# Kernel optimization log

Measured on AMD Instinct MI355X. Metric: run time of the kernel, lower is better.

## Reference

```python
import jax, jax.numpy as jnp
import numpy as np

B, S, E, H = 2, 2048, 2048, 16
D = E // H  # head_dim = 128


def setup_inputs() -> dict:
    key = jax.random.key(0)
    k1, k2, k3, k4, k5 = jax.random.split(key, 5)
    hidden_states = jax.random.normal(k1, (B, S, E), dtype=jnp.float32)
    # causal mask, broadcastable to attn_shape (B, q, H, k)
    causal = jnp.tril(jnp.ones((S, S), dtype=bool))  # [q, k]
    attention_mask = jnp.broadcast_to(causal[None, :, None, :], (B, S, 1, S))
    c_attn_w = jax.random.normal(k2, (E, E + 2 * D), dtype=jnp.float32) * (E ** -0.5)
    c_attn_b = jax.random.normal(k3, (E + 2 * D,), dtype=jnp.float32) * 0.02
    c_proj_w = jax.random.normal(k4, (E, E), dtype=jnp.float32) * (E ** -0.5)
    c_proj_b = jax.random.normal(k5, (E,), dtype=jnp.float32) * 0.02
    return {
        "hidden_states": hidden_states,
        "attention_mask": attention_mask,
        "c_attn_w": c_attn_w,
        "c_attn_b": c_attn_b,
        "c_proj_w": c_proj_w,
        "c_proj_b": c_proj_b,
    }


def reference(hidden_states, attention_mask, c_attn_w, c_attn_b, c_proj_w, c_proj_b):
    b, s, e = hidden_states.shape
    h, d = H, D
    qkv = hidden_states @ c_attn_w + c_attn_b            # [b, s, e + 2d]
    query = qkv[..., :e]                                 # [b, s, e]
    key = qkv[..., e:e + d]                              # [b, s, d] (single shared KV head)
    value = qkv[..., e + d:]                             # [b, s, d]
    scale = 1.0 / (d ** 0.5)                             # scale_attn_weights, unscale=1
    q = query.reshape(b, s * h, d)
    # QK^T with MQA broadcast: [b, s*h, k]
    scores = jnp.einsum('bqd,bkd->bqk', q, key) * scale
    scores = scores.reshape(b, s, h, s)                  # attn_shape (b, q, h, k)
    mask_value = jnp.finfo(scores.dtype).min
    scores = jnp.where(attention_mask, scores, mask_value)
    probs = jax.nn.softmax(scores, axis=-1)              # fp32 softmax (upcast is no-op in fp32)
    attn = jnp.einsum('bqk,bkd->bqd', probs.reshape(b, s * h, s), value)
    attn = attn.reshape(b, s, e)
    return attn @ c_proj_w + c_proj_b
```

## Files before the change

### kernel.cpp

```cpp
#include <hip/hip_runtime.h>
#include <math.h>


typedef __attribute__((ext_vector_type(8))) short short8;
typedef __attribute__((ext_vector_type(8))) __bf16 bf16x8;
typedef __attribute__((ext_vector_type(4))) float floatx4;
typedef __attribute__((ext_vector_type(4))) unsigned short ushort4v;
typedef unsigned short ushort;

__device__ __forceinline__ ushort f2bf(float f) {
    unsigned u = __builtin_bit_cast(unsigned, f);
    u += 0x7fffu + ((u >> 16) & 1u);
    return (ushort)(u >> 16);
}
__device__ __forceinline__ unsigned pk2(float a, float b) {
    return (unsigned)f2bf(a) | ((unsigned)f2bf(b) << 16);
}

template <typename V>
__device__ __forceinline__ auto mfma_try(V a, V b, floatx4 c, int)
    -> decltype(__builtin_amdgcn_mfma_f32_16x16x32_bf16(a, b, c, 0, 0, 0)) {
    return __builtin_amdgcn_mfma_f32_16x16x32_bf16(a, b, c, 0, 0, 0);
}
template <typename V>
__device__ __forceinline__ floatx4 mfma_try(V a, V b, floatx4 c, long) {
    return __builtin_amdgcn_mfma_f32_16x16x32_bf16(
        __builtin_bit_cast(bf16x8, a), __builtin_bit_cast(bf16x8, b), c, 0, 0, 0);
}
__device__ __forceinline__ floatx4 mfma_bf16(short8 a, short8 b, floatx4 c) {
    return mfma_try(a, b, c, 0);
}

__device__ __forceinline__ void gld_lds16(const ushort* g, ushort* l) {
    __builtin_amdgcn_global_load_lds(
        (const __attribute__((address_space(1))) unsigned*)(const void*)g,
        (__attribute__((address_space(3))) unsigned*)(void*)l, 16, 0, 0);
}

__global__ __launch_bounds__(256) void convert_bf16(const float* __restrict__ X,
                                                    ushort* __restrict__ Y, int n4) {
    int i = blockIdx.x * 256 + threadIdx.x;
    if (i >= n4) return;
    float4 v = ((const float4*)X)[i];
    ushort4v o = {f2bf(v.x), f2bf(v.y), f2bf(v.z), f2bf(v.w)};
    *(ushort4v*)&Y[(size_t)i * 4] = o;
}

__global__ __launch_bounds__(256) void transpose_convert(const float* __restrict__ W,
                                                         ushort* __restrict__ WT,
                                                         int K, int N) {
    __shared__ ushort T[64][68];
    const int tid = threadIdx.x;
    const int n0 = blockIdx.x * 64, k0 = blockIdx.y * 64;
    #pragma unroll
    for (int i = 0; i < 4; ++i) {
        int k = (tid >> 4) + i * 16, n = (tid & 15) * 4;
        float4 v = *(const float4*)&W[(size_t)(k0 + k) * N + n0 + n];
        T[n + 0][k] = f2bf(v.x); T[n + 1][k] = f2bf(v.y);
        T[n + 2][k] = f2bf(v.z); T[n + 3][k] = f2bf(v.w);
    }
    __syncthreads();
    #pragma unroll
    for (int i = 0; i < 4; ++i) {
        int idx = tid + i * 256;
        int n = idx >> 4, c4 = idx & 15;
        *(ushort4v*)&WT[(size_t)(n0 + n) * K + k0 + c4 * 4] =
            *(const ushort4v*)&T[n][c4 * 4];
    }
}

__global__ __launch_bounds__(256) void v_transpose(const ushort* __restrict__ qkv,
                                                   ushort* __restrict__ VTg) {
    __shared__ ushort T[64 * 72];
    const int tid = threadIdx.x;
    const int s0 = blockIdx.x * 64, d0 = blockIdx.y * 64, b = blockIdx.z;
    const size_t bS = (size_t)b * 2048;
    #pragma unroll
    for (int i = 0; i < 2; ++i) {
        int idx = tid + i * 256;
        int s = idx >> 3, d8 = idx & 7;
        short8 v = *(const short8*)&qkv[(bS + s0 + s) * 2304 + 2176 + d0 + d8 * 8];
        #pragma unroll
        for (int j = 0; j < 8; ++j)
            T[(d8 * 8 + j) * 72 + s] = (ushort)v[j];
    }
    __syncthreads();
    #pragma unroll
    for (int i = 0; i < 2; ++i) {
        int idx = tid + i * 256;
        int d = idx >> 3, s8 = idx & 7;
        *(short8*)&VTg[((size_t)b * 128 + d0 + d) * 2048 + s0 + s8 * 8] =
            *(const short8*)&T[d * 72 + s8 * 8];
    }
}

template <int MODE>
__global__ __launch_bounds__(256) void gemm_m97(
    const ushort* __restrict__ A, const ushort* __restrict__ BT,
    const float* __restrict__ bias, void* __restrict__ C, int M, int N, int K)
{
    __shared__ ushort As[8192];
    __shared__ ushort Bs[8192];
    const int tid = threadIdx.x, lane = tid & 63, wid = tid >> 6;
    const int wr = wid >> 1, wc = wid & 1;
    const int lg = lane >> 4, li = lane & 15;
    const int m0 = blockIdx.y * 128, n0 = blockIdx.x * 128;
    const int srow = lane >> 3;
    const int sphys = (lane & 7) * 16;
    floatx4 acc[4][4] = {};

    for (int k0 = 0; k0 < K; k0 += 64) {
        __syncthreads();
        #pragma unroll
        for (int i = 0; i < 4; ++i) {
            const int c = wid * 4 + i;
            const int row = c * 8 + srow;
            const int lin = sphys ^ ((row & 7) << 4);
            gld_lds16(&A[(size_t)(m0 + row) * K + k0 + (lin >> 1)], &As[c * 512]);
            gld_lds16(&BT[(size_t)(n0 + row) * K + k0 + (lin >> 1)], &Bs[c * 512]);
        }
        __syncthreads();
        #pragma unroll
        for (int kk = 0; kk < 2; ++kk) {
            short8 af[4], bfv[4];
            const int pb = (kk * 64 + lg * 16) ^ ((li & 7) << 4);
            #pragma unroll
            for (int m = 0; m < 4; ++m)
                af[m] = *(const short8*)&As[(wr * 64 + m * 16 + li) * 64 + (pb >> 1)];
            #pragma unroll
            for (int n = 0; n < 4; ++n)
                bfv[n] = *(const short8*)&Bs[(wc * 64 + n * 16 + li) * 64 + (pb >> 1)];
            #pragma unroll
            for (int m = 0; m < 4; ++m)
                #pragma unroll
                for (int n = 0; n < 4; ++n)
                    acc[m][n] = mfma_bf16(af[m], bfv[n], acc[m][n]);
        }
    }

    #pragma unroll
    for (int m = 0; m < 4; ++m) {
        #pragma unroll
        for (int n = 0; n < 4; ++n) {
            const int col = n0 + wc * 64 + n * 16 + li;
            const float bv = bias[col];
            #pragma unroll
            for (int r = 0; r < 4; ++r) {
                const int row = m0 + wr * 64 + m * 16 + lg * 4 + r;
                float v = acc[m][n][r] + bv;
                if constexpr (MODE == 0) {
                    if (col < 2048) v *= 0.08838834764831845f;
                    ((ushort*)C)[(size_t)row * N + col] = f2bf(v);
                } else {
                    ((float*)C)[(size_t)row * N + col] = v;
                }
            }
        }
    }
}

__global__ __launch_bounds__(256, 2) void attn_kernel(
    const ushort* __restrict__ qkv,
    const ushort* __restrict__ VTg,
    ushort* __restrict__ out)
{
    constexpr int S = 2048, Dh = 128, QKV = 2304, E = 2048;
    __shared__ ushort lds[24576];
    ushort* Ks = lds;
    ushort* VT = lds + 8192;
    ushort* Ps = lds + 16384;

    const int tid = threadIdx.x, lane = tid & 63, wid = tid >> 6;
    const int lg = lane >> 4, li = lane & 15;
    const int x = blockIdx.x;
    const int st = (x & 1) ? (x >> 1) : (15 - (x >> 1));
    const int h = blockIdx.y, b = blockIdx.z;
    const size_t bS = (size_t)b * S;
    const int qA = st * 128 + wid * 16;
    const int qB = qA + 64;

    short8 qfA[4], qfB[4];
    #pragma unroll
    for (int dc = 0; dc < 4; ++dc) {
        qfA[dc] = *(const short8*)&qkv[(bS + qA + li) * QKV + h * Dh + dc * 32 + lg * 8];
        qfB[dc] = *(const short8*)&qkv[(bS + qB + li) * QKV + h * Dh + dc * 32 + lg * 8];
    }

    floatx4 oA[8] = {}, oB[8] = {};
    float mA = -1e30f, lA = 0.f, mB = -1e30f, lB = 0.f;
    const int ntiles = 2 * st + 2;

    for (int t = 0; t < ntiles; ++t) {
        const int k0 = t * 64;
        __syncthreads();
        #pragma unroll
        for (int i = 0; i < 4; ++i) {
            const int idx = tid + i * 256;
            const int row = idx >> 4, g = idx & 15;
            const int src = (g * 16) ^ ((row & 7) << 4);
            gld_lds16(&qkv[(bS + k0 + row) * QKV + E + (src >> 1)],
                      &Ks[(i * 256 + wid * 64) * 8]);
        }
        #pragma unroll
        for (int i = 0; i < 4; ++i) {
            const int idx = tid + i * 256;
            const int d = idx >> 3, kg = idx & 7;
            gld_lds16(&VTg[((size_t)b * 128 + d) * 2048 + k0 + ((kg ^ (d & 7)) << 3)],
                      &VT[(i * 256 + wid * 64) * 8]);
        }
        __syncthreads();

        floatx4 sA[4] = {{0,0,0,0},{0,0,0,0},{0,0,0,0},{0,0,0,0}};
        floatx4 sB[4] = {{0,0,0,0},{0,0,0,0},{0,0,0,0},{0,0,0,0}};
        #pragma unroll
        for (int dc = 0; dc < 4; ++dc) {
            #pragma unroll
            for (int kb = 0; kb < 4; ++kb) {
                short8 kf = *(const short8*)&Ks[(kb * 16 + li) * 128 +
                                                (((dc * 4 + lg) ^ (li & 7)) << 3)];
                sA[kb] = mfma_bf16(kf, qfA[dc], sA[kb]);
                sB[kb] = mfma_bf16(kf, qfB[dc], sB[kb]);
            }
        }
        if (t == 2 * st) {
            #pragma unroll
            for (int kb = 0; kb < 4; ++kb)
                #pragma unroll
                for (int r = 0; r < 4; ++r)
                    if (kb * 16 + lg * 4 + r > wid * 16 + li) sA[kb][r] = -1e30f;
        }
        if (t == 2 * st + 1) {
            #pragma unroll
            for (int kb = 0; kb < 4; ++kb)
                #pragma unroll
                for (int r = 0; r < 4; ++r) {
                    sA[kb][r] = -1e30f;
                    if (kb * 16 + lg * 4 + r > wid * 16 + li) sB[kb][r] = -1e30f;
                }
        }

        {
            float mt = fmaxf(fmaxf(fmaxf(sA[0][0], sA[0][1]), fmaxf(sA[0][2], sA[0][3])),
                             fmaxf(fmaxf(sA[1][0], sA[1][1]), fmaxf(sA[1][2], sA[1][3])));
            mt = fmaxf(mt, fmaxf(fmaxf(fmaxf(sA[2][0], sA[2][1]), fmaxf(sA[2][2], sA[2][3])),
                                 fmaxf(fmaxf(sA[3][0], sA[3][1]), fmaxf(sA[3][2], sA[3][3]))));
            mt = fmaxf(mt, __shfl_xor(mt, 16));
            mt = fmaxf(mt, __shfl_xor(mt, 32));
            const float mn = fmaxf(mA, mt);
            const float sc = __expf(mA - mn);
            mA = mn;
            float rs = 0.f;
            #pragma unroll
            for (int kb = 0; kb < 4; ++kb)
                #pragma unroll
                for (int r = 0; r < 4; ++r) {
                    float p = __expf(sA[kb][r] - mn);
                    sA[kb][r] = p; rs += p;
                }
            rs += __shfl_xor(rs, 16);
            rs += __shfl_xor(rs, 32);
            lA = lA * sc + rs;
            #pragma unroll
            for (int db = 0; db < 8; ++db) oA[db] *= sc;
            #pragma unroll
            for (int kb = 0; kb < 4; ++kb) {
                const int g = kb * 2 + (lg >> 1);
                const int sw = ((g ^ (li & 7)) << 3) + ((lg & 1) * 4);
                *(unsigned*)&Ps[wid * 2048 + li * 64 + sw]     = pk2(sA[kb][0], sA[kb][1]);
                *(unsigned*)&Ps[wid * 2048 + li * 64 + sw + 2] = pk2(sA[kb][2], sA[kb][3]);
            }
        }
        {
            float mt = fmaxf(fmaxf(fmaxf(sB[0][0], sB[0][1]), fmaxf(sB[0][2], sB[0][3])),
                             fmaxf(fmaxf(sB[1][0], sB[1][1]), fmaxf(sB[1][2], sB[1][3])));
            mt = fmaxf(mt, fmaxf(fmaxf(fmaxf(sB[2][0], sB[2][1]), fmaxf(sB[2][2], sB[2][3])),
                                 fmaxf(fmaxf(sB[3][0], sB[3][1]), fmaxf(sB[3][2], sB[3][3]))));
            mt = fmaxf(mt, __shfl_xor(mt, 16));
            mt = fmaxf(mt, __shfl_xor(mt, 32));
            const float mn = fmaxf(mB, mt);
            const float sc = __expf(mB - mn);
            mB = mn;
            float rs = 0.f;
            #pragma unroll
            for (int kb = 0; kb < 4; ++kb)
                #pragma unroll
                for (int r = 0; r < 4; ++r) {
                    float p = __expf(sB[kb][r] - mn);
                    sB[kb][r] = p; rs += p;
                }
            rs += __shfl_xor(rs, 16);
            rs += __shfl_xor(rs, 32);
            lB = lB * sc + rs;
            #pragma unroll
            for (int db = 0; db < 8; ++db) oB[db] *= sc;
            #pragma unroll
            for (int kb = 0; kb < 4; ++kb) {
                const int g = kb * 2 + (lg >> 1);
                const int sw = ((g ^ (li & 7)) << 3) + ((lg & 1) * 4);
                *(unsigned*)&Ps[wid * 2048 + 1024 + li * 64 + sw]     = pk2(sB[kb][0], sB[kb][1]);
                *(unsigned*)&Ps[wid * 2048 + 1024 + li * 64 + sw + 2] = pk2(sB[kb][2], sB[kb][3]);
            }
        }

        #pragma unroll
        for (int kc = 0; kc < 2; ++kc) {
            short8 pA = *(const short8*)&Ps[wid * 2048 + li * 64 +
                                            (((kc * 4 + lg) ^ (li & 7)) << 3)];
            short8 pB = *(const short8*)&Ps[wid * 2048 + 1024 + li * 64 +
                                            (((kc * 4 + lg) ^ (li & 7)) << 3)];
            #pragma unroll
            for (int db = 0; db < 8; ++db) {
                short8 vt = *(const short8*)&VT[(db * 16 + li) * 64 +
                                                (((kc * 4 + lg) ^ (li & 7)) << 3)];
                oA[db] = mfma_bf16(vt, pA, oA[db]);
                oB[db] = mfma_bf16(vt, pB, oB[db]);
            }
        }
    }

    __syncthreads();
    ushort* Pw = lds + wid * 2176;
    {
        const float inv = 1.0f / lA;
        #pragma unroll
        for (int db = 0; db < 8; ++db) {
            *(unsigned*)&Pw[li * 136 + db * 16 + lg * 4]     = pk2(oA[db][0] * inv, oA[db][1] * inv);
            *(unsigned*)&Pw[li * 136 + db * 16 + lg * 4 + 2] = pk2(oA[db][2] * inv, oA[db][3] * inv);
        }
        #pragma unroll
        for (int i = 0; i < 4; ++i) {
            const int q = lane >> 2, d8 = (lane & 3) + i * 4;
            short8 vv = *(const short8*)&Pw[q * 136 + d8 * 8];
            *(short8*)&out[(bS + qA + q) * E + h * Dh + d8 * 8] = vv;
        }
    }
    {
        const float inv = 1.0f / lB;
        #pragma unroll
        for (int db = 0; db < 8; ++db) {
            *(unsigned*)&Pw[li * 136 + db * 16 + lg * 4]     = pk2(oB[db][0] * inv, oB[db][1] * inv);
            *(unsigned*)&Pw[li * 136 + db * 16 + lg * 4 + 2] = pk2(oB[db][2] * inv, oB[db][3] * inv);
        }
        #pragma unroll
        for (int i = 0; i < 4; ++i) {
            const int q = lane >> 2, d8 = (lane & 3) + i * 4;
            short8 vv = *(const short8*)&Pw[q * 136 + d8 * 8];
            *(short8*)&out[(bS + qB + q) * E + h * Dh + d8 * 8] = vv;
        }
    }
}

extern "C" void kernel_launch(void* const* d_in, const int* in_sizes, int n_in,
                              void* d_out, int out_size, void* d_ws, size_t ws_size,
                              hipStream_t stream) {
    (void)in_sizes; (void)n_in; (void)out_size; (void)ws_size;
    const float* hidden   = (const float*)d_in[0];
    const float* c_attn_w = (const float*)d_in[2];
    const float* c_attn_b = (const float*)d_in[3];
    const float* c_proj_w = (const float*)d_in[4];
    const float* c_proj_b = (const float*)d_in[5];
    float* outp = (float*)d_out;

    char* ws = (char*)d_ws;
    ushort* hbf  = (ushort*)ws;
    ushort* W1T  = (ushort*)(ws + (size_t)16777216);
    ushort* W2T  = (ushort*)(ws + (size_t)16777216 + 9437184);
    ushort* qkv  = (ushort*)(ws + (size_t)16777216 + 9437184 + 8388608);
    ushort* VTg  = (ushort*)(ws + (size_t)16777216 + 9437184 + 8388608 + 18874368);
    ushort* attn = hbf;

    convert_bf16<<<8192, 256, 0, stream>>>(hidden, hbf, 4096 * 2048 / 4);
    transpose_convert<<<dim3(36, 32), 256, 0, stream>>>(c_attn_w, W1T, 2048, 2304);
    transpose_convert<<<dim3(32, 32), 256, 0, stream>>>(c_proj_w, W2T, 2048, 2048);

    gemm_m97<0><<<dim3(18, 32), 256, 0, stream>>>(hbf, W1T, c_attn_b, qkv, 4096, 2304, 2048);
    v_transpose<<<dim3(32, 2, 2), 256, 0, stream>>>(qkv, VTg);
    attn_kernel<<<dim3(16, 16, 2), 256, 0, stream>>>(qkv, VTg, attn);
    gemm_m97<1><<<dim3(16, 32), 256, 0, stream>>>(attn, W2T, c_proj_b, outp, 4096, 2048, 2048);
}
```

Baseline: 239.7 us.

## Double-buffer K/V tiles with async prefetch, lazy rescale, and MFMA priority

The attention loop now double-buffers the K and V^T tiles in LDS and issues the global-to-LDS loads for tile t+1 before computing tile t, waiting only on the older loads via vmcnt. This is meant to hide global load latency behind MFMA work. It also skips the online-softmax rescale of the accumulators when no lane's running max increases, raises wave priority around the MFMA blocks, and merges two 32-bit P stores into one 64-bit store. LDS use grows from 48KB to 80KB per block, which may limit occupancy at 2 blocks per CU.

```diff
diff --git a/kernel.cpp b/kernel.cpp
--- a/kernel.cpp
+++ b/kernel.cpp
@@ -6,6 +6,7 @@
 typedef __attribute__((ext_vector_type(8))) __bf16 bf16x8;
 typedef __attribute__((ext_vector_type(4))) float floatx4;
 typedef __attribute__((ext_vector_type(4))) unsigned short ushort4v;
+typedef __attribute__((ext_vector_type(2))) unsigned uint2v;
 typedef unsigned short ushort;
 
 __device__ __forceinline__ ushort f2bf(float f) {
@@ -159,16 +160,39 @@
     }
 }
 
+#define STAGE_KV(t_, Kdst, Vdst)                                               \
+    {                                                                          \
+        const int k0_ = (t_) * 64;                                             \
+        _Pragma("unroll")                                                      \
+        for (int i_ = 0; i_ < 4; ++i_) {                                       \
+            const int idx_ = tid + i_ * 256;                                   \
+            const int row_ = idx_ >> 4, g_ = idx_ & 15;                        \
+            const int src_ = (g_ * 16) ^ ((row_ & 7) << 4);                    \
+            gld_lds16(&qkv[(bS + k0_ + row_) * QKV + E + (src_ >> 1)],         \
+                      &(Kdst)[(i_ * 256 + wid * 64) * 8]);                     \
+        }                                                                      \
+        _Pragma("unroll")                                                      \
+        for (int i_ = 0; i_ < 4; ++i_) {                                       \
+            const int idx_ = tid + i_ * 256;                                   \
+            const int d_ = idx_ >> 3, kg_ = idx_ & 7;                          \
+            gld_lds16(&VTg[((size_t)b * 128 + d_) * 2048 + k0_ +               \
+                           ((kg_ ^ (d_ & 7)) << 3)],                           \
+                      &(Vdst)[(i_ * 256 + wid * 64) * 8]);                     \
+        }                                                                      \
+    }
+
 __global__ __launch_bounds__(256, 2) void attn_kernel(
     const ushort* __restrict__ qkv,
     const ushort* __restrict__ VTg,
     ushort* __restrict__ out)
 {
     constexpr int S = 2048, Dh = 128, QKV = 2304, E = 2048;
-    __shared__ ushort lds[24576];
-    ushort* Ks = lds;
-    ushort* VT = lds + 8192;
-    ushort* Ps = lds + 16384;
+    __shared__ ushort lds[40960];
+    ushort* Ks0 = lds;
+    ushort* Ks1 = lds + 8192;
+    ushort* VT0 = lds + 16384;
+    ushort* VT1 = lds + 24576;
+    ushort* Ps  = lds + 32768;
 
     const int tid = threadIdx.x, lane = tid & 63, wid = tid >> 6;
     const int lg = lane >> 4, li = lane & 15;
@@ -190,38 +214,38 @@
     float mA = -1e30f, lA = 0.f, mB = -1e30f, lB = 0.f;
     const int ntiles = 2 * st + 2;
 
+    STAGE_KV(0, Ks0, VT0);
+
     for (int t = 0; t < ntiles; ++t) {
-        const int k0 = t * 64;
         __syncthreads();
-        #pragma unroll
-        for (int i = 0; i < 4; ++i) {
-            const int idx = tid + i * 256;
-            const int row = idx >> 4, g = idx & 15;
-            const int src = (g * 16) ^ ((row & 7) << 4);
-            gld_lds16(&qkv[(bS + k0 + row) * QKV + E + (src >> 1)],
-                      &Ks[(i * 256 + wid * 64) * 8]);
-        }
-        #pragma unroll
-        for (int i = 0; i < 4; ++i) {
-            const int idx = tid + i * 256;
-            const int d = idx >> 3, kg = idx & 7;
-            gld_lds16(&VTg[((size_t)b * 128 + d) * 2048 + k0 + ((kg ^ (d & 7)) << 3)],
-                      &VT[(i * 256 + wid * 64) * 8]);
-        }
+        ushort* Kcur = (t & 1) ? Ks1 : Ks0;
+        ushort* Vcur = (t & 1) ? VT1 : VT0;
+        if (t + 1 < ntiles) {
+            ushort* Knxt = (t & 1) ? Ks0 : Ks1;
+            ushort* Vnxt = (t & 1) ? VT0 : VT1;
+            STAGE_KV(t + 1, Knxt, Vnxt);
+            asm volatile("s_waitcnt vmcnt(8)" ::: "memory");
+        } else {
+            asm volatile("s_waitcnt vmcnt(0)" ::: "memory");
+        }
+        __builtin_amdgcn_sched_barrier(0);
         __syncthreads();
 
         floatx4 sA[4] = {{0,0,0,0},{0,0,0,0},{0,0,0,0},{0,0,0,0}};
         floatx4 sB[4] = {{0,0,0,0},{0,0,0,0},{0,0,0,0},{0,0,0,0}};
+        __builtin_amdgcn_s_setprio(1);
         #pragma unroll
         for (int dc = 0; dc < 4; ++dc) {
             #pragma unroll
             for (int kb = 0; kb < 4; ++kb) {
-                short8 kf = *(const short8*)&Ks[(kb * 16 + li) * 128 +
-                                                (((dc * 4 + lg) ^ (li & 7)) << 3)];
+                short8 kf = *(const short8*)&Kcur[(kb * 16 + li) * 128 +
+                                                  (((dc * 4 + lg) ^ (li & 7)) << 3)];
                 sA[kb] = mfma_bf16(kf, qfA[dc], sA[kb]);
                 sB[kb] = mfma_bf16(kf, qfB[dc], sB[kb]);
             }
         }
+        __builtin_amdgcn_s_setprio(0);
+
         if (t == 2 * st) {
             #pragma unroll
             for (int kb = 0; kb < 4; ++kb)
@@ -246,28 +270,31 @@
                                  fmaxf(fmaxf(sA[3][0], sA[3][1]), fmaxf(sA[3][2], sA[3][3]))));
             mt = fmaxf(mt, __shfl_xor(mt, 16));
             mt = fmaxf(mt, __shfl_xor(mt, 32));
-            const float mn = fmaxf(mA, mt);
-            const float sc = __expf(mA - mn);
-            mA = mn;
+            if (!__all(mt <= mA)) {
+                const float mn = fmaxf(mA, mt);
+                const float sc = __expf(mA - mn);
+                mA = mn;
+                lA *= sc;
+                #pragma unroll
+                for (int db = 0; db < 8; ++db) oA[db] *= sc;
+            }
             float rs = 0.f;
             #pragma unroll
             for (int kb = 0; kb < 4; ++kb)
                 #pragma unroll
                 for (int r = 0; r < 4; ++r) {
-                    float p = __expf(sA[kb][r] - mn);
+                    float p = __expf(sA[kb][r] - mA);
                     sA[kb][r] = p; rs += p;
                 }
             rs += __shfl_xor(rs, 16);
             rs += __shfl_xor(rs, 32);
-            lA = lA * sc + rs;
-            #pragma unroll
-            for (int db = 0; db < 8; ++db) oA[db] *= sc;
+            lA += rs;
             #pragma unroll
             for (int kb = 0; kb < 4; ++kb) {
                 const int g = kb * 2 + (lg >> 1);
                 const int sw = ((g ^ (li & 7)) << 3) + ((lg & 1) * 4);
-                *(unsigned*)&Ps[wid * 2048 + li * 64 + sw]     = pk2(sA[kb][0], sA[kb][1]);
-                *(unsigned*)&Ps[wid * 2048 + li * 64 + sw + 2] = pk2(sA[kb][2], sA[kb][3]);
+                uint2v w = {pk2(sA[kb][0], sA[kb][1]), pk2(sA[kb][2], sA[kb][3])};
+                *(uint2v*)&Ps[wid * 2048 + li * 64 + sw] = w;
             }
         }
         {
@@ -277,31 +304,35 @@
                                  fmaxf(fmaxf(sB[3][0], sB[3][1]), fmaxf(sB[3][2], sB[3][3]))));
             mt = fmaxf(mt, __shfl_xor(mt, 16));
             mt = fmaxf(mt, __shfl_xor(mt, 32));
-            const float mn = fmaxf(mB, mt);
-            const float sc = __expf(mB - mn);
-            mB = mn;
+            if (!__all(mt <= mB)) {
+                const float mn = fmaxf(mB, mt);
+                const float sc = __expf(mB - mn);
+                mB = mn;
+                lB *= sc;
+                #pragma unroll
+                for (int db = 0; db < 8; ++db) oB[db] *= sc;
+            }
             float rs = 0.f;
             #pragma unroll
             for (int kb = 0; kb < 4; ++kb)
                 #pragma unroll
                 for (int r = 0; r < 4; ++r) {
-                    float p = __expf(sB[kb][r] - mn);
+                    float p = __expf(sB[kb][r] - mB);
                     sB[kb][r] = p; rs += p;
                 }
             rs += __shfl_xor(rs, 16);
             rs += __shfl_xor(rs, 32);
-            lB = lB * sc + rs;
-            #pragma unroll
-            for (int db = 0; db < 8; ++db) oB[db] *= sc;
+            lB += rs;
             #pragma unroll
             for (int kb = 0; kb < 4; ++kb) {
                 const int g = kb * 2 + (lg >> 1);
                 const int sw = ((g ^ (li & 7)) << 3) + ((lg & 1) * 4);
-                *(unsigned*)&Ps[wid * 2048 + 1024 + li * 64 + sw]     = pk2(sB[kb][0], sB[kb][1]);
-                *(unsigned*)&Ps[wid * 2048 + 1024 + li * 64 + sw + 2] = pk2(sB[kb][2], sB[kb][3]);
-            }
-        }
-
+                uint2v w = {pk2(sB[kb][0], sB[kb][1]), pk2(sB[kb][2], sB[kb][3])};
+                *(uint2v*)&Ps[wid * 2048 + 1024 + li * 64 + sw] = w;
+            }
+        }
+
+        __builtin_amdgcn_s_setprio(1);
         #pragma unroll
         for (int kc = 0; kc < 2; ++kc) {
             short8 pA = *(const short8*)&Ps[wid * 2048 + li * 64 +
@@ -310,12 +341,13 @@
                                             (((kc * 4 + lg) ^ (li & 7)) << 3)];
             #pragma unroll
             for (int db = 0; db < 8; ++db) {
-                short8 vt = *(const short8*)&VT[(db * 16 + li) * 64 +
-                                                (((kc * 4 + lg) ^ (li & 7)) << 3)];
+                short8 vt = *(const short8*)&Vcur[(db * 16 + li) * 64 +
+                                                  (((kc * 4 + lg) ^ (li & 7)) << 3)];
                 oA[db] = mfma_bf16(vt, pA, oA[db]);
                 oB[db] = mfma_bf16(vt, pB, oB[db]);
             }
         }
+        __builtin_amdgcn_s_setprio(0);
     }
 
     __syncthreads();
```

New measurement: 243.5 us. Within noise of the previous version (+1.6%).
